# Kernel optimization log

Measured on AMD Instinct MI355X. Metric: run time of the kernel, lower is better.

## Reference

```python
import jax, jax.numpy as jnp
import numpy as np

EPSILON = 0.1   # EpsilonNN threshold
TOPK = 30       # KNN k
NORM_EPS = 1e-12  # F.normalize eps


def setup_inputs() -> dict:
    key = jax.random.key(0)
    k1, k2 = jax.random.split(key)
    context = jax.random.normal(k1, (4096, 512), dtype=jnp.float32)
    weight = jax.random.normal(k2, (16, 512), dtype=jnp.float32)  # (num_pers, input_size)
    return {"context": context, "weight": weight}


def reference(context, weight):
    # WeightedCosine: per-perspective reweighting + L2 normalize + mean cosine
    P = weight.shape[0]
    cf = context[None, :, :] * weight[:, None, :]                    # (P, N, d)
    norm = jnp.maximum(jnp.linalg.norm(cf, axis=-1, keepdims=True), NORM_EPS)
    cn = cf / norm                                                   # (P, N, d)
    # mean over perspectives of cn @ cn.T, contracted in one einsum
    att = jnp.einsum('pnd,pmd->nm', cn, cn) / P                      # (N, N)
    # EpsilonNN: zero out entries <= epsilon
    att = jnp.where(att > EPSILON, att, jnp.zeros((), att.dtype))
    # KNN: keep top-k per row, zero elsewhere
    N = att.shape[0]
    _, idx = jax.lax.top_k(att, TOPK)                                # (N, k)
    mask = jnp.zeros_like(att).at[jnp.arange(N)[:, None], idx].set(1.0)
    return att * mask
```

## Files before the change

kernel.cpp:

```cpp
#include <hip/hip_runtime.h>
#include <math.h>
#include <stdint.h>

#define N_CTX 4096
#define DIM 512
#define NPERS 16
#define KTOT (NPERS * DIM)
#define EPS_NN 0.1f
#define TOPK_K 30

#define DELTA 4e-4f
#define DELTA2 1e-5f
#define CAP 64
#define CAPL 12

#define BM 128
#define BK 64
#define NKSTEP (KTOT / BK)
#define CHUNK 16384

typedef __attribute__((ext_vector_type(8))) short bfrag;
typedef __attribute__((ext_vector_type(4))) float f32x4;

__device__ __forceinline__ unsigned short f2bf(float f) {
  unsigned u = __float_as_uint(f);
  unsigned r = u + 0x7FFFu + ((u >> 16) & 1u);
  return (unsigned short)(r >> 16);
}

#define SWZ(r, b) ((b) ^ (((r) & 7) << 4))

__device__ __forceinline__ void stage1k(const char* gsrc, char* ldst, int lane) {
#if __has_builtin(__builtin_amdgcn_global_load_lds)
  __builtin_amdgcn_global_load_lds(
      (const __attribute__((address_space(1))) unsigned int*)(uintptr_t)(gsrc + lane * 16),
      (__attribute__((address_space(3))) unsigned int*)(uintptr_t)ldst, 16, 0, 0);
#else
  *reinterpret_cast<uint4*>(ldst + lane * 16) =
      *reinterpret_cast<const uint4*>(gsrc + lane * 16);
#endif
}

__global__ __launch_bounds__(256) void norms_kernel(
    const float* __restrict__ ctx, const float* __restrict__ w,
    float* __restrict__ invr, int* __restrict__ gcount) {
  int wid = threadIdx.x >> 6;
  int lane = threadIdx.x & 63;
  int gid = blockIdx.x * 4 + wid;
  if (blockIdx.x == 0 && threadIdx.x == 0) gcount[0] = 0;
  int p = gid >> 12;
  int n = gid & (N_CTX - 1);
  const float4* c4 = reinterpret_cast<const float4*>(ctx + (size_t)n * DIM + lane * 8);
  const float4* w4 = reinterpret_cast<const float4*>(w + (size_t)p * DIM + lane * 8);
  float4 c0 = c4[0], c1 = c4[1];
  float4 w0 = w4[0], w1 = w4[1];
  float s = 0.f, v;
  v = c0.x * w0.x; s = fmaf(v, v, s);
  v = c0.y * w0.y; s = fmaf(v, v, s);
  v = c0.z * w0.z; s = fmaf(v, v, s);
  v = c0.w * w0.w; s = fmaf(v, v, s);
  v = c1.x * w1.x; s = fmaf(v, v, s);
  v = c1.y * w1.y; s = fmaf(v, v, s);
  v = c1.z * w1.z; s = fmaf(v, v, s);
  v = c1.w * w1.w; s = fmaf(v, v, s);
#pragma unroll
  for (int off = 32; off; off >>= 1) s += __shfl_down(s, off, 64);
  if (lane == 0) invr[(size_t)p * N_CTX + n] = 0.25f / fmaxf(sqrtf(s), 1e-12f);
}

__global__ __launch_bounds__(256) void split_norms_kernel(
    const float* __restrict__ ctx, const float* __restrict__ w,
    float* __restrict__ invr, unsigned short* __restrict__ Fhi,
    int* __restrict__ gcount) {
  const int tid = blockIdx.x * 256 + threadIdx.x;
  if (tid == 0) gcount[0] = 0;
  const int n = tid >> 6;
  const int db = tid & 63;
  const int d0 = db * 8;
  const int P = n >> 7;
  const int r = n & 127;
  const int sl = db & 7;
  const int swzoff = r * 128 + ((sl * 16) ^ ((r & 7) << 4));

  const float4 c0 = *reinterpret_cast<const float4*>(ctx + (size_t)n * DIM + d0);
  const float4 c1 = *reinterpret_cast<const float4*>(ctx + (size_t)n * DIM + d0 + 4);

#pragma unroll
  for (int p = 0; p < NPERS; ++p) {
    const float4 w0 = *reinterpret_cast<const float4*>(w + (size_t)p * DIM + d0);
    const float4 w1 = *reinterpret_cast<const float4*>(w + (size_t)p * DIM + d0 + 4);

    float pr[8] = {c0.x * w0.x, c0.y * w0.y, c0.z * w0.z, c0.w * w0.w,
                   c1.x * w1.x, c1.y * w1.y, c1.z * w1.z, c1.w * w1.w};

    float s = 0.f;
#pragma unroll
    for (int j = 0; j < 8; ++j) s = fmaf(pr[j], pr[j], s);
#pragma unroll
    for (int off = 32; off; off >>= 1) s += __shfl_down(s, off, 64);
    const float stot = __shfl(s, 0, 64);
    const float sc = 0.25f / fmaxf(sqrtf(stot), 1e-12f);
    if (db == 0) invr[(size_t)p * N_CTX + n] = sc;

    unsigned hb[8];
#pragma unroll
    for (int j = 0; j < 8; ++j) hb[j] = f2bf(pr[j] * sc);
    uint4 hv = make_uint4(hb[0] | (hb[1] << 16), hb[2] | (hb[3] << 16),
                          hb[4] | (hb[5] << 16), hb[6] | (hb[7] << 16));
    const int kstep = p * 8 + (db >> 3);
    const size_t base = (size_t)(P * 128 + kstep) * CHUNK + swzoff;
    *reinterpret_cast<uint4*>((char*)Fhi + base) = hv;
  }
}

__global__ __launch_bounds__(256, 3) void att_gemm_fast(
    const unsigned short* __restrict__ Fhi, float* __restrict__ out) {
  const int bid0 = blockIdx.x;
  int bid = (bid0 & 7) * 66 + (bid0 >> 3);
  int by = 0;
  while (bid >= (by + 1) * 32 - ((by + 1) * by) / 2) ++by;
  const int bx = by + (bid - (by * 32 - (by * (by - 1)) / 2));

  __shared__ __align__(16) char Ahi[CHUNK];
  __shared__ __align__(16) char Bhi[CHUNK];

  const int t = threadIdx.x;
  const int lane = t & 63, wid = t >> 6;
  const int wr = wid >> 1, wc = wid & 1;
  const int woff = __builtin_amdgcn_readfirstlane(wid * 4096);

  const char* gAh = (const char*)Fhi + (size_t)by * NKSTEP * CHUNK + woff;
  const char* gBh = (const char*)Fhi + (size_t)bx * NKSTEP * CHUNK + woff;

  f32x4 acc[4][4] = {};

  for (int s = 0; s < NKSTEP; ++s) {
    const size_t so = (size_t)s * CHUNK;
#pragma unroll
    for (int i = 0; i < 4; ++i) {
      stage1k(gAh + so + i * 1024, Ahi + woff + i * 1024, lane);
      stage1k(gBh + so + i * 1024, Bhi + woff + i * 1024, lane);
    }
    __syncthreads();

#pragma unroll
    for (int ks = 0; ks < 2; ++ks) {
      const int kb = ks * 64 + (lane >> 4) * 16;
      bfrag ah[4], bh[4];
#pragma unroll
      for (int m = 0; m < 4; ++m) {
        const int r = wr * 64 + m * 16 + (lane & 15);
        ah[m] = *reinterpret_cast<const bfrag*>(Ahi + r * 128 + SWZ(r, kb));
      }
#pragma unroll
      for (int n2 = 0; n2 < 4; ++n2) {
        const int r = wc * 64 + n2 * 16 + (lane & 15);
        bh[n2] = *reinterpret_cast<const bfrag*>(Bhi + r * 128 + SWZ(r, kb));
      }
#pragma unroll
      for (int m = 0; m < 4; ++m)
#pragma unroll
        for (int n2 = 0; n2 < 4; ++n2)
          acc[m][n2] = __builtin_amdgcn_mfma_f32_16x16x32_bf16(ah[m], bh[n2], acc[m][n2], 0, 0, 0);
    }
    __syncthreads();
  }

  const int Ro = by * BM, Co = bx * BM;
  const int col = lane & 15, rq = (lane >> 4) * 4;
#pragma unroll
  for (int m = 0; m < 4; ++m)
#pragma unroll
    for (int n2 = 0; n2 < 4; ++n2) {
      const int gr = Ro + wr * 64 + m * 16 + rq;
      const int gc = Co + wc * 64 + n2 * 16 + col;
#pragma unroll
      for (int j = 0; j < 4; ++j)
        out[(size_t)(gr + j) * N_CTX + gc] = acc[m][n2][j];
      if (bx != by) {
        *reinterpret_cast<float4*>(out + (size_t)gc * N_CTX + gr) =
            make_float4(acc[m][n2][0], acc[m][n2][1], acc[m][n2][2], acc[m][n2][3]);
      }
    }
}

__device__ __forceinline__ void stage_half(char* __restrict__ hi_base,
                                           char* __restrict__ lo_base,
                                           const float4* cv, const float4* wv,
                                           float s, int r, int h) {
  unsigned hu[16], lu[16];
#pragma unroll
  for (int i = 0; i < 8; ++i) {
    float f[4] = {cv[i].x * wv[i].x * s, cv[i].y * wv[i].y * s,
                  cv[i].z * wv[i].z * s, cv[i].w * wv[i].w * s};
    unsigned hb[4], lb[4];
#pragma unroll
    for (int j = 0; j < 4; ++j) {
      hb[j] = f2bf(f[j]);
      float hf = __uint_as_float(hb[j] << 16);
      lb[j] = f2bf(f[j] - hf);
    }
    hu[2 * i] = hb[0] | (hb[1] << 16);
    hu[2 * i + 1] = hb[2] | (hb[3] << 16);
    lu[2 * i] = lb[0] | (lb[1] << 16);
    lu[2 * i + 1] = lb[2] | (lb[3] << 16);
  }
#pragma unroll
  for (int c = 0; c < 4; ++c) {
    int boff = r * 128 + SWZ(r, h * 64 + c * 16);
    *reinterpret_cast<uint4*>(hi_base + boff) =
        make_uint4(hu[4 * c], hu[4 * c + 1], hu[4 * c + 2], hu[4 * c + 3]);
    *reinterpret_cast<uint4*>(lo_base + boff) =
        make_uint4(lu[4 * c], lu[4 * c + 1], lu[4 * c + 2], lu[4 * c + 3]);
  }
}

__global__ __launch_bounds__(256, 2) void att_gemm(
    const float* __restrict__ ctx, const float* __restrict__ w,
    const float* __restrict__ invr, float* __restrict__ out) {
  const int bx = blockIdx.x, by = blockIdx.y;
  if (by > bx) return;

  __shared__ __align__(16) char Ahi[BM * 128];
  __shared__ __align__(16) char Alo[BM * 128];
  __shared__ __align__(16) char Bhi[BM * 128];
  __shared__ __align__(16) char Blo[BM * 128];

  const int t = threadIdx.x;
  const int lane = t & 63, wid = t >> 6;
  const int wr = wid >> 1, wc = wid & 1;
  const int Ro = by * BM, Co = bx * BM;
  const int srow = t >> 1;
  const int sh = t & 1;

  f32x4 acc[4][4] = {};

  for (int k0 = 0; k0 < KTOT; k0 += BK) {
    const int p = k0 >> 9;
    const int d0 = (k0 & (DIM - 1)) + sh * 32;

    float4 cva[8], cvb[8], wv[8];
    const float* wrow = w + (size_t)p * DIM + d0;
    const float* arow = ctx + (size_t)(Ro + srow) * DIM + d0;
    const float* brow = ctx + (size_t)(Co + srow) * DIM + d0;
#pragma unroll
    for (int i = 0; i < 8; ++i) {
      wv[i] = *reinterpret_cast<const float4*>(wrow + 4 * i);
      cva[i] = *reinterpret_cast<const float4*>(arow + 4 * i);
      cvb[i] = *reinterpret_cast<const float4*>(brow + 4 * i);
    }
    const float sA = invr[(size_t)p * N_CTX + Ro + srow];
    const float sB = invr[(size_t)p * N_CTX + Co + srow];

    __syncthreads();
    stage_half(Ahi, Alo, cva, wv, sA, srow, sh);
    stage_half(Bhi, Blo, cvb, wv, sB, srow, sh);
    __syncthreads();

#pragma unroll
    for (int ks = 0; ks < 2; ++ks) {
      const int kb = ks * 64 + (lane >> 4) * 16;
      bfrag ah[4], al[4], bh[4], bl[4];
#pragma unroll
      for (int m = 0; m < 4; ++m) {
        const int r = wr * 64 + m * 16 + (lane & 15);
        const int off = r * 128 + SWZ(r, kb);
        ah[m] = *reinterpret_cast<const bfrag*>(Ahi + off);
        al[m] = *reinterpret_cast<const bfrag*>(Alo + off);
      }
#pragma unroll
      for (int n = 0; n < 4; ++n) {
        const int r = wc * 64 + n * 16 + (lane & 15);
        const int off = r * 128 + SWZ(r, kb);
        bh[n] = *reinterpret_cast<const bfrag*>(Bhi + off);
        bl[n] = *reinterpret_cast<const bfrag*>(Blo + off);
      }
#pragma unroll
      for (int m = 0; m < 4; ++m)
#pragma unroll
        for (int n = 0; n < 4; ++n) {
          acc[m][n] = __builtin_amdgcn_mfma_f32_16x16x32_bf16(ah[m], bh[n], acc[m][n], 0, 0, 0);
          acc[m][n] = __builtin_amdgcn_mfma_f32_16x16x32_bf16(ah[m], bl[n], acc[m][n], 0, 0, 0);
          acc[m][n] = __builtin_amdgcn_mfma_f32_16x16x32_bf16(al[m], bh[n], acc[m][n], 0, 0, 0);
        }
    }
  }

  const int col = lane & 15, rq = (lane >> 4) * 4;
#pragma unroll
  for (int m = 0; m < 4; ++m)
#pragma unroll
    for (int n = 0; n < 4; ++n) {
      const int gr = Ro + wr * 64 + m * 16 + rq;
      const int gc = Co + wc * 64 + n * 16 + col;
#pragma unroll
      for (int j = 0; j < 4; ++j)
        out[(size_t)(gr + j) * N_CTX + gc] = acc[m][n][j];
      if (bx != by) {
        *reinterpret_cast<float4*>(out + (size_t)gc * N_CTX + gr) =
            make_float4(acc[m][n][0], acc[m][n][1], acc[m][n][2], acc[m][n][3]);
      }
    }
}

__global__ __launch_bounds__(256) void topk_scan(
    float* __restrict__ att, int* __restrict__ candM,
    float* __restrict__ candV, int* __restrict__ cnt_g) {
  __shared__ unsigned red[2][4];
  __shared__ int lcnt, lg;

  const int n = blockIdx.x;
  const int t = threadIdx.x;
  const int wid = t >> 6, lane = t & 63;
  float* row = att + (size_t)n * N_CTX;

  float ar[16], tr[16];
  unsigned ur[16];
#pragma unroll
  for (int i = 0; i < 4; ++i) {
    float4 v4 = *reinterpret_cast<const float4*>(row + (size_t)(i * 256 + t) * 4);
    float tmp[4] = {v4.x, v4.y, v4.z, v4.w};
#pragma unroll
    for (int j = 0; j < 4; ++j) {
      float a = tmp[j];
      float tt = (a > EPS_NN) ? a : 0.0f;
      ar[i * 4 + j] = a;
      tr[i * 4 + j] = tt;
      ur[i * 4 + j] = __float_as_uint(tt);
    }
  }
  if (t == 0) { lcnt = 0; lg = 0; }

  unsigned lo = 0u, hi = 0x7F800000u;
  int buf = 0;
  while (lo < hi) {
    unsigned mid = lo + ((hi - lo) >> 1);
    unsigned c = 0;
#pragma unroll
    for (int i = 0; i < 16; ++i) c += (ur[i] > mid) ? 1u : 0u;
#pragma unroll
    for (int off = 32; off; off >>= 1) c += __shfl_down(c, off, 64);
    if (lane == 0) red[buf][wid] = c;
    __syncthreads();
    unsigned tot = red[buf][0] + red[buf][1] + red[buf][2] + red[buf][3];
    if (tot < TOPK_K) hi = mid; else lo = mid + 1;
    buf ^= 1;
  }
  const float vk = __uint_as_float(lo);
  const bool nearEps = (vk <= EPS_NN + 2.0f * DELTA);
  __syncthreads();

  unsigned myg = 0;
#pragma unroll
  for (int i = 0; i < 16; ++i) {
    const int blk = i >> 2, j = i & 3;
    const int m = (blk * 256 + t) * 4 + j;
    const float a = ar[i], tt = tr[i];
    const bool isEps = fabsf(a - EPS_NN) <= DELTA;
    const bool isOrd = (tt > 0.f) && (fabsf(tt - vk) <= DELTA);
    const bool cand = isOrd || (isEps && nearEps);
    const bool defIn = (tt > vk + DELTA) && !cand;
    tr[i] = defIn ? tt : 0.f;
    myg += defIn ? 1u : 0u;
    unsigned long long mask = __ballot(cand);
    if (mask) {
      int base = 0;
      if (lane == 0) base = atomicAdd(&lcnt, (int)__popcll(mask));
      base = __shfl(base, 0, 64);
      if (cand) {
        int pos = base + (int)__popcll(mask & ((1ull << lane) - 1ull));
        if (pos < CAP) {
          candM[n * CAP + pos] = m;
          candV[n * CAP + pos] = tt;
        }
      }
    }
  }
#pragma unroll
  for (int off = 32; off; off >>= 1) myg += __shfl_down(myg, off, 64);
  if (lane == 0) atomicAdd(&lg, (int)myg);

#pragma unroll
  for (int i = 0; i < 4; ++i) {
    *reinterpret_cast<float4*>(row + (size_t)(i * 256 + t) * 4) =
        make_float4(tr[i * 4], tr[i * 4 + 1], tr[i * 4 + 2], tr[i * 4 + 3]);
  }
  __syncthreads();
  if (t == 0) {
    cnt_g[4 * n] = (lcnt < CAP) ? lcnt : CAP;
    cnt_g[4 * n + 1] = lg;
    cnt_g[4 * n + 2] = nearEps ? 1 : 0;
  }
}

__global__ __launch_bounds__(64) void repair_select(
    const float* __restrict__ ctx, const float* __restrict__ w,
    const float* __restrict__ invr, const int* __restrict__ candM,
    const float* __restrict__ candV, const int* __restrict__ cnt_g,
    int* __restrict__ glist, int* __restrict__ gcount,
    float* __restrict__ att) {
  const int n = blockIdx.x;
  const int c = cnt_g[4 * n];
  if (c == 0) return;
  const int slots = TOPK_K - cnt_g[4 * n + 1];
  const int nearEps = cnt_g[4 * n + 2];
  const int j = threadIdx.x;

  if (c <= slots && !nearEps) {
    if (j < c) att[(size_t)n * N_CTX + candM[n * CAP + j]] = candV[n * CAP + j];
    return;
  }

  __shared__ int m_s[CAP];
  __shared__ float rv_s[CAP];
  __shared__ float rr_s[CAP];
  if (j < c) m_s[j] = candM[n * CAP + j];
  __syncthreads();

  const float* cn = ctx + (size_t)n * DIM;
  for (int q = 0; q < c; ++q) {
    const int mq = m_s[q];
    const float* cm = ctx + (size_t)mq * DIM;
    float acc8[8] = {0.f, 0.f, 0.f, 0.f, 0.f, 0.f, 0.f, 0.f};
    for (int p = 0; p < NPERS; ++p) {
      const float sA = invr[(size_t)p * N_CTX + n];
      const float sB = invr[(size_t)p * N_CTX + mq];
      const float* wp = w + (size_t)p * DIM;
#pragma unroll
      for (int i2 = 0; i2 < 8; ++i2) {
        const int d = j + 64 * i2;
        const float fa = (cn[d] * wp[d]) * sA;
        const float fb = (cm[d] * wp[d]) * sB;
        acc8[i2] = fmaf(fa, fb, acc8[i2]);
      }
    }
    float part = ((acc8[0] + acc8[1]) + (acc8[2] + acc8[3])) +
                 ((acc8[4] + acc8[5]) + (acc8[6] + acc8[7]));
#pragma unroll
    for (int off = 32; off; off >>= 1) part += __shfl_down(part, off, 64);
    if (j == 0) {
      rr_s[q] = part;
      rv_s[q] = (part > EPS_NN) ? part : 0.f;
    }
  }
  __syncthreads();

  bool kept = false;
  float rv = 0.f, rr = 0.f;
  if (j < c) {
    rv = rv_s[j];
    rr = rr_s[j];
    const int m = m_s[j];
    int rank = 0;
    for (int i = 0; i < c; ++i) {
      if (i == j) continue;
      rank += ((rv_s[i] > rv) || (rv_s[i] == rv && m_s[i] < m)) ? 1 : 0;
    }
    kept = (rank < slots);
  }
  float mk = (j < c && kept) ? rv : 3.4e38f;
  float mo = (j < c && !kept) ? rv : -3.4e38f;
  float ea = (j < c && fabsf(rr - EPS_NN) <= DELTA2) ? 1.f : 0.f;
#pragma unroll
  for (int off = 32; off; off >>= 1) {
    mk = fminf(mk, __shfl_down(mk, off, 64));
    mo = fmaxf(mo, __shfl_down(mo, off, 64));
    ea = fmaxf(ea, __shfl_down(ea, off, 64));
  }
  mk = __shfl(mk, 0, 64);
  mo = __shfl(mo, 0, 64);
  ea = __shfl(ea, 0, 64);
  const bool ambiguous = (mk - mo <= DELTA2) || (ea > 0.f);

  if (ambiguous) {
    if (j == 0) {
      int gp = atomicAdd(gcount, 1);
      glist[gp] = n;
    }
    return;
  }
  if (j < c && kept) att[(size_t)n * N_CTX + m_s[j]] = rv;
}

__global__ __launch_bounds__(64) void repair_chain(
    const float* __restrict__ ctx, const float* __restrict__ w,
    const float* __restrict__ invr, const int* __restrict__ candM,
    const int* __restrict__ cnt_g, const int* __restrict__ glist,
    const int* __restrict__ gcount, float* __restrict__ att) {
  if (blockIdx.x >= gcount[0]) return;
  const int n = glist[blockIdx.x];
  const int c = cnt_g[4 * n];
  const int slots = TOPK_K - cnt_g[4 * n + 1];
  const int j = threadIdx.x;

  __shared__ __align__(16) float wL[KTOT];
  __shared__ __align__(16) float cnL[DIM];
  __shared__ __align__(16) float cmL[CAPL][516];
  __shared__ float te_s[CAP];
  __shared__ int m_s[CAP];

  if (j < c) m_s[j] = candM[n * CAP + j];
  __syncthreads();

  {
    const float4* wg = reinterpret_cast<const float4*>(w);
    float4* wl = reinterpret_cast<float4*>(wL);
#pragma unroll
    for (int i = 0; i < 32; ++i) wl[i * 64 + j] = wg[i * 64 + j];
    const float4* cg = reinterpret_cast<const float4*>(ctx + (size_t)n * DIM);
    float4* cl = reinterpret_cast<float4*>(cnL);
#pragma unroll
    for (int i = 0; i < 2; ++i) cl[i * 64 + j] = cg[i * 64 + j];
    const int cl2 = (c < CAPL) ? c : CAPL;
    for (int r = 0; r < cl2; ++r) {
      const float4* mg = reinterpret_cast<const float4*>(ctx + (size_t)m_s[r] * DIM);
      float4* ml = reinterpret_cast<float4*>(&cmL[r][0]);
#pragma unroll
      for (int i = 0; i < 2; ++i) ml[i * 64 + j] = mg[i * 64 + j];
    }
  }
  __syncthreads();

  float te = -1.f;
  int m = -1;
  if (j < c) {
    m = m_s[j];
    const float4* cn4 = reinterpret_cast<const float4*>(cnL);
    const float4* cm4 = (j < CAPL)
        ? reinterpret_cast<const float4*>(&cmL[j][0])
        : reinterpret_cast<const float4*>(ctx + (size_t)m * DIM);
    float e = 0.f;
    for (int p = 0; p < NPERS; ++p) {
      const float sA = invr[(size_t)p * N_CTX + n];
      const float sB = invr[(size_t)p * N_CTX + m];
      const float4* w4 = reinterpret_cast<const float4*>(wL + p * DIM);
#pragma unroll 4
      for (int q = 0; q < DIM / 4; ++q) {
        const float4 a = cn4[q], b = cm4[q], ww = w4[q];
        e = fmaf((a.x * ww.x) * sA, (b.x * ww.x) * sB, e);
        e = fmaf((a.y * ww.y) * sA, (b.y * ww.y) * sB, e);
        e = fmaf((a.z * ww.z) * sA, (b.z * ww.z) * sB, e);
        e = fmaf((a.w * ww.w) * sA, (b.w * ww.w) * sB, e);
      }
    }
    te = (e > EPS_NN) ? e : 0.f;
  }
  te_s[j] = te;
  __syncthreads();
  if (j < c) {
    int rank = 0;
    for (int i = 0; i < c; ++i) {
      if (i == j) continue;
      rank += ((te_s[i] > te) || (te_s[i] == te && m_s[i] < m)) ? 1 : 0;
    }
    if (rank < slots) att[(size_t)n * N_CTX + m] = te;
  }
}

extern "C" void kernel_launch(void* const* d_in, const int* in_sizes, int n_in,
                              void* d_out, int out_size, void* d_ws, size_t ws_size,
                              hipStream_t stream) {
  const float* ctx = (const float*)d_in[0];
  const float* w   = (const float*)d_in[1];
  float* out = (float*)d_out;

  const size_t OFF_CNT = 262144;
  const size_t OFF_CAND = OFF_CNT + 65536;
  const size_t OFF_CV = OFF_CAND + 1048576;
  const size_t OFF_GL = OFF_CV + 1048576;
  const size_t OFF_GC = OFF_GL + 16384;
  const size_t OFF_FHI = OFF_GC + 4096;
  const size_t FSZ = (size_t)32 * NKSTEP * CHUNK;
  float* invr = (float*)d_ws;
  int* cnt_g = (int*)((char*)d_ws + OFF_CNT);
  int* candM = (int*)((char*)d_ws + OFF_CAND);
  float* candV = (float*)((char*)d_ws + OFF_CV);
  int* glist = (int*)((char*)d_ws + OFF_GL);
  int* gcount = (int*)((char*)d_ws + OFF_GC);
  unsigned short* Fhi = (unsigned short*)((char*)d_ws + OFF_FHI);
  const bool haveF = ws_size >= OFF_FHI + FSZ;

  if (haveF) {
    split_norms_kernel<<<(N_CTX * 64) / 256, 256, 0, stream>>>(ctx, w, invr, Fhi, gcount);
    att_gemm_fast<<<528, 256, 0, stream>>>(Fhi, out);
  } else {
    norms_kernel<<<(NPERS * N_CTX) / 4, 256, 0, stream>>>(ctx, w, invr, gcount);
    dim3 grid(N_CTX / BM, N_CTX / BM);
    att_gemm<<<grid, 256, 0, stream>>>(ctx, w, invr, out);
  }

  topk_scan<<<N_CTX, 256, 0, stream>>>(out, candM, candV, cnt_g);
  repair_select<<<N_CTX, 64, 0, stream>>>(ctx, w, invr, candM, candV, cnt_g,
                                          glist, gcount, out);
  repair_chain<<<N_CTX, 64, 0, stream>>>(ctx, w, invr, candM, cnt_g,
                                         glist, gcount, out);
}
```

Before: 409.6 us.

## Emit sparse above-threshold candidate lists from GEMM instead of dense attention matrix

The GEMM epilogue stops writing the full dense 4096x4096 similarity matrix. It appends only entries above epsilon minus a margin to per-row lists, using atomic counters with a fixed capacity. A new select_compact kernel does the top-k selection and exact fp32 repair from these short lists, replacing the dense topk_scan and repair_select passes. The output is zeroed with a memset, so the large dense write and re-read are replaced by one memset and sparse scatters. The risk is silent truncation when a row has more than 256 candidates, plus atomic contention in the epilogue.

```diff
diff --git a/kernel.cpp b/kernel.cpp
--- a/kernel.cpp
+++ b/kernel.cpp
@@ -13,6 +13,7 @@
 #define DELTA2 1e-5f
 #define CAP 64
 #define CAPL 12
+#define RCAP 256
 
 #define BM 128
 #define BK 64
@@ -71,9 +72,10 @@
 __global__ __launch_bounds__(256) void split_norms_kernel(
     const float* __restrict__ ctx, const float* __restrict__ w,
     float* __restrict__ invr, unsigned short* __restrict__ Fhi,
-    int* __restrict__ gcount) {
+    int* __restrict__ gcount, int* __restrict__ rcnt) {
   const int tid = blockIdx.x * 256 + threadIdx.x;
   if (tid == 0) gcount[0] = 0;
+  if (tid < N_CTX) rcnt[tid] = 0;
   const int n = tid >> 6;
   const int db = tid & 63;
   const int d0 = db * 8;
@@ -114,7 +116,8 @@
 }
 
 __global__ __launch_bounds__(256, 3) void att_gemm_fast(
-    const unsigned short* __restrict__ Fhi, float* __restrict__ out) {
+    const unsigned short* __restrict__ Fhi, int* __restrict__ rcnt,
+    int* __restrict__ rlistM, float* __restrict__ rlistV) {
   const int bid0 = blockIdx.x;
   int bid = (bid0 & 7) * 66 + (bid0 >> 3);
   int by = 0;
@@ -168,6 +171,7 @@
 
   const int Ro = by * BM, Co = bx * BM;
   const int col = lane & 15, rq = (lane >> 4) * 4;
+  const float TH = EPS_NN - DELTA;
 #pragma unroll
   for (int m = 0; m < 4; ++m)
 #pragma unroll
@@ -175,11 +179,22 @@
       const int gr = Ro + wr * 64 + m * 16 + rq;
       const int gc = Co + wc * 64 + n2 * 16 + col;
 #pragma unroll
-      for (int j = 0; j < 4; ++j)
-        out[(size_t)(gr + j) * N_CTX + gc] = acc[m][n2][j];
-      if (bx != by) {
-        *reinterpret_cast<float4*>(out + (size_t)gc * N_CTX + gr) =
-            make_float4(acc[m][n2][0], acc[m][n2][1], acc[m][n2][2], acc[m][n2][3]);
+      for (int j = 0; j < 4; ++j) {
+        const float v = acc[m][n2][j];
+        if (v > TH) {
+          int pos = atomicAdd(&rcnt[gr + j], 1);
+          if (pos < RCAP) {
+            rlistM[(size_t)(gr + j) * RCAP + pos] = gc;
+            rlistV[(size_t)(gr + j) * RCAP + pos] = v;
+          }
+          if (bx != by) {
+            int pos2 = atomicAdd(&rcnt[gc], 1);
+            if (pos2 < RCAP) {
+              rlistM[(size_t)gc * RCAP + pos2] = gr + j;
+              rlistV[(size_t)gc * RCAP + pos2] = v;
+            }
+          }
+        }
       }
     }
 }
@@ -482,6 +497,167 @@
   if (j < c && kept) att[(size_t)n * N_CTX + m_s[j]] = rv;
 }
 
+__global__ __launch_bounds__(64) void select_compact(
+    const float* __restrict__ ctx, const float* __restrict__ w,
+    const float* __restrict__ invr, const int* __restrict__ rcnt,
+    const int* __restrict__ rlistM, const float* __restrict__ rlistV,
+    int* __restrict__ candM, int* __restrict__ cnt_g,
+    int* __restrict__ glist, int* __restrict__ gcount,
+    float* __restrict__ att) {
+  const int n = blockIdx.x;
+  const int j = threadIdx.x;
+  int nc = rcnt[n];
+  if (nc > RCAP) nc = RCAP;
+  if (nc == 0) return;
+
+  __shared__ int mL[RCAP];
+  __shared__ float vL[RCAP];
+  __shared__ float ttL[RCAP];
+  __shared__ int cM[CAP];
+  __shared__ float cV[CAP];
+  __shared__ int lc;
+  if (j == 0) lc = 0;
+  for (int i = j; i < nc; i += 64) {
+    const float a = rlistV[(size_t)n * RCAP + i];
+    mL[i] = rlistM[(size_t)n * RCAP + i];
+    vL[i] = a;
+    ttL[i] = (a > EPS_NN) ? a : 0.f;
+  }
+  __syncthreads();
+
+  float vkLoc = 3.4e38f;
+  int posLoc = 0;
+  float ttOwn[4];
+  int gtOwn[4];
+#pragma unroll
+  for (int s = 0; s < 4; ++s) { ttOwn[s] = -1.f; gtOwn[s] = 0; }
+#pragma unroll
+  for (int s = 0; s < 4; ++s) {
+    const int idx = j + s * 64;
+    if (idx < nc) {
+      const float t = ttL[idx];
+      ttOwn[s] = t;
+      posLoc += (t > 0.f) ? 1 : 0;
+      int g = 0;
+      for (int i = 0; i < nc; ++i) g += (ttL[i] > t) ? 1 : 0;
+      gtOwn[s] = g;
+      if (t > 0.f && g <= TOPK_K - 1) vkLoc = fminf(vkLoc, t);
+    }
+  }
+#pragma unroll
+  for (int off = 32; off; off >>= 1) {
+    posLoc += __shfl_down(posLoc, off, 64);
+    vkLoc = fminf(vkLoc, __shfl_down(vkLoc, off, 64));
+  }
+  const int pos = __shfl(posLoc, 0, 64);
+  float vk = __shfl(vkLoc, 0, 64);
+  if (pos < TOPK_K) vk = 0.f;
+  const bool nearEps = (vk <= EPS_NN + 2.0f * DELTA);
+
+  int gLoc = 0;
+#pragma unroll
+  for (int s = 0; s < 4; ++s) {
+    const int idx = j + s * 64;
+    if (idx < nc) {
+      const float a = vL[idx], tt = ttOwn[s];
+      const bool isEps = fabsf(a - EPS_NN) <= DELTA;
+      const bool isOrd = (tt > 0.f) && (fabsf(tt - vk) <= DELTA);
+      const bool cand = isOrd || (isEps && nearEps);
+      const bool defIn = (tt > vk + DELTA) && !cand;
+      if (defIn) {
+        att[(size_t)n * N_CTX + mL[idx]] = tt;
+        ++gLoc;
+      }
+      if (cand) {
+        int p2 = atomicAdd(&lc, 1);
+        if (p2 < CAP) { cM[p2] = mL[idx]; cV[p2] = tt; }
+      }
+    }
+  }
+#pragma unroll
+  for (int off = 32; off; off >>= 1) gLoc += __shfl_down(gLoc, off, 64);
+  const int g = __shfl(gLoc, 0, 64);
+  __syncthreads();
+  int c = lc;
+  if (c > CAP) c = CAP;
+  if (c == 0) return;
+  const int slots = TOPK_K - g;
+
+  if (c <= slots && !nearEps) {
+    if (j < c) att[(size_t)n * N_CTX + cM[j]] = cV[j];
+    return;
+  }
+
+  __shared__ float rv_s[CAP];
+  __shared__ float rr_s[CAP];
+  const float* cn = ctx + (size_t)n * DIM;
+  for (int q = 0; q < c; ++q) {
+    const int mq = cM[q];
+    const float* cm = ctx + (size_t)mq * DIM;
+    float acc8[8] = {0.f, 0.f, 0.f, 0.f, 0.f, 0.f, 0.f, 0.f};
+    for (int p = 0; p < NPERS; ++p) {
+      const float sA = invr[(size_t)p * N_CTX + n];
+      const float sB = invr[(size_t)p * N_CTX + mq];
+      const float* wp = w + (size_t)p * DIM;
+#pragma unroll
+      for (int i2 = 0; i2 < 8; ++i2) {
+        const int d = j + 64 * i2;
+        const float fa = (cn[d] * wp[d]) * sA;
+        const float fb = (cm[d] * wp[d]) * sB;
+        acc8[i2] = fmaf(fa, fb, acc8[i2]);
+      }
+    }
+    float part = ((acc8[0] + acc8[1]) + (acc8[2] + acc8[3])) +
+                 ((acc8[4] + acc8[5]) + (acc8[6] + acc8[7]));
+#pragma unroll
+    for (int off = 32; off; off >>= 1) part += __shfl_down(part, off, 64);
+    if (j == 0) {
+      rr_s[q] = part;
+      rv_s[q] = (part > EPS_NN) ? part : 0.f;
+    }
+  }
+  __syncthreads();
+
+  bool kept = false;
+  float rv = 0.f, rr = 0.f;
+  if (j < c) {
+    rv = rv_s[j];
+    rr = rr_s[j];
+    const int m = cM[j];
+    int rank = 0;
+    for (int i = 0; i < c; ++i) {
+      if (i == j) continue;
+      rank += ((rv_s[i] > rv) || (rv_s[i] == rv && cM[i] < m)) ? 1 : 0;
+    }
+    kept = (rank < slots);
+  }
+  float mk = (j < c && kept) ? rv : 3.4e38f;
+  float mo = (j < c && !kept) ? rv : -3.4e38f;
+  float ea = (j < c && fabsf(rr - EPS_NN) <= DELTA2) ? 1.f : 0.f;
+#pragma unroll
+  for (int off = 32; off; off >>= 1) {
+    mk = fminf(mk, __shfl_down(mk, off, 64));
+    mo = fmaxf(mo, __shfl_down(mo, off, 64));
+    ea = fmaxf(ea, __shfl_down(ea, off, 64));
+  }
+  mk = __shfl(mk, 0, 64);
+  mo = __shfl(mo, 0, 64);
+  ea = __shfl(ea, 0, 64);
+  const bool ambiguous = (mk - mo <= DELTA2) || (ea > 0.f);
+
+  if (ambiguous) {
+    if (j < c) candM[n * CAP + j] = cM[j];
+    if (j == 0) {
+      cnt_g[4 * n] = c;
+      cnt_g[4 * n + 1] = g;
+      int gp = atomicAdd(gcount, 1);
+      glist[gp] = n;
+    }
+    return;
+  }
+  if (j < c && kept) att[(size_t)n * N_CTX + cM[j]] = rv;
+}
+
 __global__ __launch_bounds__(64) void repair_chain(
     const float* __restrict__ ctx, const float* __restrict__ w,
     const float* __restrict__ invr, const int* __restrict__ candM,
@@ -569,7 +745,10 @@
   const size_t OFF_CV = OFF_CAND + 1048576;
   const size_t OFF_GL = OFF_CV + 1048576;
   const size_t OFF_GC = OFF_GL + 16384;
-  const size_t OFF_FHI = OFF_GC + 4096;
+  const size_t OFF_RC = OFF_GC + 4096;
+  const size_t OFF_RM = OFF_RC + 16384;
+  const size_t OFF_RV = OFF_RM + 4194304;
+  const size_t OFF_FHI = OFF_RV + 4194304;
   const size_t FSZ = (size_t)32 * NKSTEP * CHUNK;
   float* invr = (float*)d_ws;
   int* cnt_g = (int*)((char*)d_ws + OFF_CNT);
@@ -577,21 +756,29 @@
   float* candV = (float*)((char*)d_ws + OFF_CV);
   int* glist = (int*)((char*)d_ws + OFF_GL);
   int* gcount = (int*)((char*)d_ws + OFF_GC);
+  int* rcnt = (int*)((char*)d_ws + OFF_RC);
+  int* rlistM = (int*)((char*)d_ws + OFF_RM);
+  float* rlistV = (float*)((char*)d_ws + OFF_RV);
   unsigned short* Fhi = (unsigned short*)((char*)d_ws + OFF_FHI);
   const bool haveF = ws_size >= OFF_FHI + FSZ;
 
+  hipMemsetAsync(out, 0, (size_t)N_CTX * N_CTX * sizeof(float), stream);
+
   if (haveF) {
-    split_norms_kernel<<<(N_CTX * 64) / 256, 256, 0, stream>>>(ctx, w, invr, Fhi, gcount);
-    att_gemm_fast<<<528, 256, 0, stream>>>(Fhi, out);
+    split_norms_kernel<<<(N_CTX * 64) / 256, 256, 0, stream>>>(ctx, w, invr, Fhi,
+                                                               gcount, rcnt);
+    att_gemm_fast<<<528, 256, 0, stream>>>(Fhi, rcnt, rlistM, rlistV);
+    select_compact<<<N_CTX, 64, 0, stream>>>(ctx, w, invr, rcnt, rlistM, rlistV,
+                                             candM, cnt_g, glist, gcount, out);
   } else {
     norms_kernel<<<(NPERS * N_CTX) / 4, 256, 0, stream>>>(ctx, w, invr, gcount);
     dim3 grid(N_CTX / BM, N_CTX / BM);
     att_gemm<<<grid, 256, 0, stream>>>(ctx, w, invr, out);
-  }
-
-  topk_scan<<<N_CTX, 256, 0, stream>>>(out, candM, candV, cnt_g);
-  repair_select<<<N_CTX, 64, 0, stream>>>(ctx, w, invr, candM, candV, cnt_g,
-                                          glist, gcount, out);
+    topk_scan<<<N_CTX, 256, 0, stream>>>(out, candM, candV, cnt_g);
+    repair_select<<<N_CTX, 64, 0, stream>>>(ctx, w, invr, candM, candV, cnt_g,
+                                            glist, gcount, out);
+  }
+
   repair_chain<<<N_CTX, 64, 0, stream>>>(ctx, w, invr, candM, cnt_g,
                                          glist, gcount, out);
 }
```

New measurement: 399.9 us. 2.4% less time.
